# Kernel optimization log

Hardware: AMD Instinct MI355X
Metric: run time of the kernel (lower is better)

Reference implementation:

```python
import jax, jax.numpy as jnp
import numpy as np
import math

DIM = 2048
NUM_HEADS = 16
HEAD_DIM = DIM // NUM_HEADS
SEQ = 2048
BATCH = 4
THETA = 10000.0


def _rope_tables(seq_len, d, theta):
    # faithful to RotaryEmbedding: emb = cat([freqs, freqs], -1), then [..., ::2]
    inv_freq = 1.0 / theta ** (np.arange(0, d, 2, dtype=np.float32) / d)  # [d/2]
    t = np.arange(seq_len, dtype=np.float32)
    freqs = np.einsum('i,j->ij', t, inv_freq)          # [S, d/2]
    emb = np.concatenate([freqs, freqs], axis=-1)       # [S, d]
    cos_split = np.cos(emb)[:, ::2]                     # [S, d/2]
    sin_split = np.sin(emb)[:, ::2]                     # [S, d/2]
    return jnp.asarray(cos_split), jnp.asarray(sin_split)


def _apply_rope(x, cos_s, sin_s):
    # x: [b, h, s, d]; cos_s/sin_s: [s, d/2]
    x1 = x[..., ::2]
    x2 = x[..., 1::2]
    c = cos_s[None, None]
    s = sin_s[None, None]
    return jnp.concatenate([x1 * c - x2 * s, x1 * s + x2 * c], axis=-1)


def setup_inputs() -> dict:
    key = jax.random.key(0)
    k1, k2, k3 = jax.random.split(key, 3)
    x = jax.random.normal(k1, (BATCH, SEQ, DIM), dtype=jnp.float32)
    # causal additive mask [1,1,S,S]
    neg = jnp.finfo(jnp.float32).min
    causal = jnp.tril(jnp.ones((SEQ, SEQ), dtype=bool))
    mask = jnp.where(causal, 0.0, neg)[None, None].astype(jnp.float32)
    w_qkv = jax.random.normal(k2, (3 * DIM, DIM), dtype=jnp.float32) * (1.0 / math.sqrt(DIM))
    w_out = jax.random.normal(k3, (DIM, DIM), dtype=jnp.float32) * (1.0 / math.sqrt(DIM))
    return {"x": x, "mask": mask, "w_qkv": w_qkv, "w_out": w_out}


def reference(x, mask, w_qkv, w_out):
    b, s, _ = x.shape
    h, d = NUM_HEADS, HEAD_DIM
    qkv = jnp.einsum('bse,fe->bsf', x, w_qkv)           # [b, s, 3*dim]
    q, k, v = jnp.split(qkv, 3, axis=-1)
    # b s (h d) -> b h s d
    reshp = lambda t: t.reshape(b, s, h, d).transpose(0, 2, 1, 3)
    q, k, v = reshp(q), reshp(k), reshp(v)
    cos_s, sin_s = _rope_tables(s, d, THETA)
    q = _apply_rope(q, cos_s, sin_s)
    k = _apply_rope(k, cos_s, sin_s)
    att = jnp.einsum('bhqd,bhkd->bhqk', q, k) / math.sqrt(d)
    att = att + mask
    att = jax.nn.softmax(att, axis=-1)
    y = jnp.einsum('bhqk,bhkd->bhqd', att, v)           # [b, h, s, d]
    y = y.transpose(0, 2, 1, 3).reshape(b, s, h * d)
    return jnp.einsum('bse,fe->bsf', y, w_out)
```

## Files before the change

### kernel.cpp

```cpp
#include <hip/hip_runtime.h>

typedef unsigned short u16;
typedef unsigned int u32;
typedef __attribute__((ext_vector_type(4))) float f32x4;
typedef __attribute__((ext_vector_type(16))) float f32x16;
typedef __attribute__((ext_vector_type(8))) short bf16x8;
typedef __attribute__((ext_vector_type(4))) float float4v;
typedef __attribute__((ext_vector_type(4))) unsigned short u16x4;
typedef __attribute__((ext_vector_type(8))) unsigned short u16x8;

__device__ __forceinline__ float bf2f(u16 u) { return __uint_as_float(((u32)u) << 16); }
__device__ __forceinline__ u16 f2bf(float f) {
  u32 x = __float_as_uint(f);
  x += 0x7fffu + ((x >> 16) & 1u);
  return (u16)(x >> 16);
}
__device__ __forceinline__ u32 cvtpk(float lo, float hi_) {
  u32 r;
  asm("v_cvt_pk_bf16_f32 %0, %1, %2" : "=v"(r) : "v"(lo), "v"(hi_));
  return r;
}

__device__ __forceinline__ void gll16(const void* g, void* l) {
  __builtin_amdgcn_global_load_lds((const __attribute__((address_space(1))) void*)g,
                                   (__attribute__((address_space(3))) void*)l, 16, 0, 0);
}

#define MFMA_BF16(a, b, c) __builtin_amdgcn_mfma_f32_16x16x32_bf16((a), (b), (c), 0, 0, 0)
#define MFMA32(a, b, c) __builtin_amdgcn_mfma_f32_32x32x16_bf16((a), (b), (c), 0, 0, 0)

#define BARRIER() __builtin_amdgcn_s_barrier()
#define LGKM0() do { asm volatile("s_waitcnt lgkmcnt(0)" ::: "memory"); \
                     __builtin_amdgcn_sched_barrier(0); } while (0)
#define VMCNT(n) do { asm volatile("s_waitcnt vmcnt(" #n ")" ::: "memory"); \
                      __builtin_amdgcn_sched_barrier(0); } while (0)

__global__ __launch_bounds__(256) void cast_kernel(const float* __restrict__ src,
                                                   u16* __restrict__ dst, int n) {
  const int stride = gridDim.x * 256 * 4;
  for (int i = (blockIdx.x * 256 + threadIdx.x) * 4; i < n; i += stride) {
    const float4v v = *(const float4v*)(src + i);
    u16x4 o;
    o[0] = f2bf(v[0]); o[1] = f2bf(v[1]); o[2] = f2bf(v[2]); o[3] = f2bf(v[3]);
    *(u16x4*)(dst + i) = o;
  }
}

__global__ __launch_bounds__(256) void rope_tables(float* __restrict__ cosd,
                                                   float* __restrict__ sind) {
  const int idx = blockIdx.x * 256 + threadIdx.x;
  const int t = idx >> 6, j = idx & 63;
  const float inv = powf(10000.0f, -(float)(j & 31) * (1.0f / 32.0f));
  const float ang = (float)t * inv;
  cosd[idx] = cosf(ang);
  sind[idx] = sinf(ang);
}

__device__ __forceinline__ void store_out(float* C, size_t i, float v) { C[i] = v; }
__device__ __forceinline__ void store_out(u16* C, size_t i, float v) { C[i] = f2bf(v); }

#define PH_MFMA(MG, NG)                                                          \
  do {                                                                           \
    _Pragma("unroll") for (int i_ = 0; i_ < 4; ++i_)                             \
      _Pragma("unroll") for (int jn_ = 0; jn_ < 2; ++jn_)                        \
        _Pragma("unroll") for (int ks_ = 0; ks_ < 2; ++ks_)                      \
          acc[(MG) * 4 + i_][(NG) * 2 + jn_] =                                   \
              MFMA_BF16(af[i_][ks_], bfr[jn_][ks_],                              \
                        acc[(MG) * 4 + i_][(NG) * 2 + jn_]);                     \
  } while (0)

template <typename OutT>
__global__ __launch_bounds__(512, 2) void gemm_bt8(const u16* __restrict__ A,
                                                   const u16* __restrict__ B,
                                                   OutT* __restrict__ C, int M, int N, int K,
                                                   int lda, int ldb, int ldc) {
  __shared__ __align__(16) u16 LDS[2][2][2][128 * 64];
  const int nbn = N >> 8;
  const int nwg = gridDim.x;
  const int wg = (blockIdx.x & 7) * (nwg >> 3) + (blockIdx.x >> 3);
  const int bm = wg / nbn, bn = wg % nbn;
  const int tid = threadIdx.x;
  const int w = tid >> 6, l = tid & 63, l15 = l & 15, l4 = l >> 4;
  const int wr = w >> 2, wc = w & 3;
  const u16* Abase = A + (size_t)bm * 256 * lda;
  const u16* Bbase = B + (size_t)bn * 256 * ldb;
  const int NT = K >> 6;

  f32x4 acc[8][4] = {};
  bf16x8 af[4][2], bfr[2][2];

  auto STAGE = [&](int sel, int h, int t) {
    const u16* src = (sel ? Bbase + (size_t)h * 128 * ldb : Abase + (size_t)h * 128 * lda) +
                     t * 64;
    const int ld = sel ? ldb : lda;
    char* dst = (char*)&LDS[t & 1][sel][h][0];
#pragma unroll
    for (int j = 0; j < 2; ++j) {
      const int o = j * 8192 + tid * 16;
      const int r = o >> 7;
      const int cb = (o & 127) ^ ((r & 7) << 4);
      gll16(src + (size_t)r * ld + (cb >> 1), dst + o);
    }
  };
  auto LDA_ = [&](int bb, int mg) {
    const char* base = (const char*)&LDS[bb][0][mg][0];
#pragma unroll
    for (int i = 0; i < 4; ++i) {
      const int R = i * 32 + wr * 16 + l15;
#pragma unroll
      for (int ks = 0; ks < 2; ++ks)
        af[i][ks] = *(const bf16x8*)(base + R * 128 + ((ks * 64 + l4 * 16) ^ ((R & 7) << 4)));
    }
  };
  auto LDB_ = [&](int bb, int ng) {
    const char* base = (const char*)&LDS[bb][1][ng][0];
#pragma unroll
    for (int jn = 0; jn < 2; ++jn) {
      const int R = jn * 64 + wc * 16 + l15;
#pragma unroll
      for (int ks = 0; ks < 2; ++ks)
        bfr[jn][ks] = *(const bf16x8*)(base + R * 128 + ((ks * 64 + l4 * 16) ^ ((R & 7) << 4)));
    }
  };

  STAGE(0, 0, 0); STAGE(1, 0, 0); STAGE(0, 1, 0); STAGE(1, 1, 0);
  if (NT > 1) { STAGE(1, 0, 1); STAGE(0, 1, 1); STAGE(1, 1, 1); }
  VMCNT(6);
  BARRIER();

  for (int T = 0; T < NT; ++T) {
    const int bb = T & 1;
    LDA_(bb, 0); LDB_(bb, 0);
    if (T + 1 < NT) STAGE(0, 0, T + 1);
    BARRIER(); LGKM0();
    __builtin_amdgcn_s_setprio(1); PH_MFMA(0, 0); __builtin_amdgcn_s_setprio(0);
    BARRIER();
    LDA_(bb, 1);
    if (T + 2 < NT) STAGE(1, 0, T + 2);
    BARRIER(); LGKM0();
    __builtin_amdgcn_s_setprio(1); PH_MFMA(1, 0); __builtin_amdgcn_s_setprio(0);
    BARRIER();
    LDB_(bb, 1);
    if (T + 2 < NT) STAGE(0, 1, T + 2);
    BARRIER(); LGKM0();
    __builtin_amdgcn_s_setprio(1); PH_MFMA(1, 1); __builtin_amdgcn_s_setprio(0);
    BARRIER();
    LDA_(bb, 0);
    if (T + 2 < NT) STAGE(1, 1, T + 2);
    BARRIER(); LGKM0();
    __builtin_amdgcn_s_setprio(1); PH_MFMA(0, 1); __builtin_amdgcn_s_setprio(0);
    if (T + 2 < NT) { VMCNT(6); } else { VMCNT(0); }
    BARRIER();
  }

#pragma unroll
  for (int mf = 0; mf < 8; ++mf) {
    const int mg = mf >> 2, i = mf & 3;
    const int row0 = bm * 256 + mg * 128 + i * 32 + wr * 16 + l4 * 4;
#pragma unroll
    for (int f = 0; f < 4; ++f) {
      const int col = bn * 256 + f * 64 + wc * 16 + l15;
#pragma unroll
      for (int rr = 0; rr < 4; ++rr)
        store_out(C, (size_t)(row0 + rr) * ldc + col, acc[mf][f][rr]);
    }
  }
}

__global__ __launch_bounds__(256) void rope_apply_inplace(u16* __restrict__ qkvb,
                                                          const float* __restrict__ cosd,
                                                          const float* __restrict__ sind) {
  const int wid = blockIdx.x * 4 + (threadIdx.x >> 6);
  const int j = threadIdx.x & 63;
  const int h = wid & 15;
  const int m = wid >> 4;
  const int s = m & 2047;
  const float c = cosd[s * 64 + j];
  const float sn = sind[s * 64 + j];
  u16* qp = qkvb + (size_t)m * 6144 + h * 128;
  u16* kp = qp + 2048;
  const u32 qv = *(const u32*)(qp + 2 * j);
  const u32 kv = *(const u32*)(kp + 2 * j);
  const float q1 = bf2f((u16)(qv & 0xffff)), q2 = bf2f((u16)(qv >> 16));
  const float k1 = bf2f((u16)(kv & 0xffff)), k2 = bf2f((u16)(kv >> 16));
  qp[j]      = f2bf(q1 * c - q2 * sn);
  qp[64 + j] = f2bf(q1 * sn + q2 * c);
  kp[j]      = f2bf(k1 * c - k2 * sn);
  kp[64 + j] = f2bf(k1 * sn + k2 * c);
}

__global__ __launch_bounds__(256) void v_transpose(const u16* __restrict__ qkvb,
                                                   u16* __restrict__ vt) {
  __shared__ u16 tile[64][130];
  const int st = blockIdx.x & 31, bh = blockIdx.x >> 5;
  const int b = bh >> 4, h = bh & 15;
  const int tid = threadIdx.x;
#pragma unroll
  for (int p = 0; p < 4; ++p) {
    const int ss = p * 16 + (tid >> 4);
    const int d0 = (tid & 15) * 8;
    const u16x8 v = *(const u16x8*)(qkvb + (size_t)(b * 2048 + st * 64 + ss) * 6144 +
                                    4096 + h * 128 + d0);
#pragma unroll
    for (int i = 0; i < 8; ++i) tile[ss][d0 + i] = v[i];
  }
  __syncthreads();
#pragma unroll
  for (int p = 0; p < 4; ++p) {
    const int d = p * 32 + (tid >> 3);
    const int s0 = (tid & 7) * 8;
    u16x8 ov;
#pragma unroll
    for (int i = 0; i < 8; ++i) ov[i] = tile[s0 + i][d];
    *(u16x8*)(vt + (size_t)(bh * 128 + d) * 2048 + st * 64 + s0) = ov;
  }
}

__global__ __launch_bounds__(512, 2) void flash_attn(u16* __restrict__ qkvb,
                                                     const u16* __restrict__ vt) {
  __shared__ __align__(16) char smem[65536];
  const int bh = blockIdx.x;
  const int qt = 7 - blockIdx.y;
  const int b = bh >> 4, h = bh & 15;
  const int tid = threadIdx.x;
  const int w = tid >> 6, l = tid & 63;
  const int l31 = l & 31, hi = l >> 5;

  const int q0 = qt * 256 + w * 32;
  const int qg = q0 + l31;

  bf16x8 qf[8];
  {
    const u16* Qrow = qkvb + (size_t)(b * 2048 + qg) * 6144 + h * 128 + hi * 8;
#pragma unroll
    for (int d = 0; d < 8; ++d) qf[d] = *(const bf16x8*)(Qrow + d * 16);
  }

  f32x16 ot[4];
#pragma unroll
  for (int dt = 0; dt < 4; ++dt) ot[dt] = 0.f;
  float mrun = -1e30f, lrun = 0.f;

  const int NT = 4 * qt + 4;
  const u16* Kg0 = qkvb + (size_t)b * 2048 * 6144 + 2048 + h * 128;
  const u16* Vg0 = vt + (size_t)bh * 128 * 2048;

  auto STAGE = [&](int t) {
    const u16* Kg = Kg0 + (size_t)t * 64 * 6144;
    const u16* Vg = Vg0 + t * 64;
    char* kd = smem + (t & 1) * 16384;
    char* vd = smem + 32768 + (t & 1) * 16384;
#pragma unroll
    for (int j = 0; j < 2; ++j) {
      const int o = j * 8192 + tid * 16;
      {
        const int r = o >> 8;
        const int cb = (o & 255) ^ ((r & 15) << 4);
        gll16(Kg + (size_t)r * 6144 + (cb >> 1), kd + o);
      }
      {
        const int r = o >> 7;
        const int cb = (o & 127) ^ ((r & 7) << 4);
        gll16(Vg + (size_t)r * 2048 + (cb >> 1), vd + o);
      }
    }
  };

  STAGE(0);
  VMCNT(0);
  BARRIER();

  for (int kt = 0; kt < NT; ++kt) {
    if (kt + 1 < NT) STAGE(kt + 1);

    if (kt * 64 <= q0 + 31) {
      const char* Kb = smem + (kt & 1) * 16384;
      const char* Vb = smem + 32768 + (kt & 1) * 16384;

      f32x16 sa[2];
      sa[0] = 0.f; sa[1] = 0.f;
#pragma unroll
      for (int ks2 = 0; ks2 < 2; ++ks2) {
        const int R = ks2 * 32 + l31;
#pragma unroll
        for (int d = 0; d < 8; ++d) {
          const bf16x8 kf = *(const bf16x8*)(Kb + R * 256 +
                                             ((d * 32 + hi * 16) ^ ((R & 15) << 4)));
          sa[ks2] = MFMA32(kf, qf[d], sa[ks2]);
        }
      }

      const float SCALE = 0.08838834764831845f;
      float tmax = -1e30f;
      if (kt * 64 + 63 > q0) {
#pragma unroll
        for (int ks2 = 0; ks2 < 2; ++ks2)
#pragma unroll
          for (int rg = 0; rg < 16; ++rg) {
            const int key = kt * 64 + ks2 * 32 + (rg & 3) + 8 * (rg >> 2) + 4 * hi;
            float sv = sa[ks2][rg] * SCALE;
            sv = (key > qg) ? -1e30f : sv;
            sa[ks2][rg] = sv;
            tmax = fmaxf(tmax, sv);
          }
      } else {
#pragma unroll
        for (int ks2 = 0; ks2 < 2; ++ks2)
#pragma unroll
          for (int rg = 0; rg < 16; ++rg) {
            const float sv = sa[ks2][rg] * SCALE;
            sa[ks2][rg] = sv;
            tmax = fmaxf(tmax, sv);
          }
      }
      tmax = fmaxf(tmax, __shfl_xor(tmax, 32));

      const float mnew = fmaxf(mrun, tmax);
      const float alpha = __expf(mrun - mnew);
      mrun = mnew;
      float rsum = 0.f;
#pragma unroll
      for (int ks2 = 0; ks2 < 2; ++ks2)
#pragma unroll
        for (int rg = 0; rg < 16; ++rg) {
          const float pv = __expf(sa[ks2][rg] - mnew);
          sa[ks2][rg] = pv;
          rsum += pv;
        }
      rsum += __shfl_xor(rsum, 32);
      lrun = lrun * alpha + rsum;
#pragma unroll
      for (int dt = 0; dt < 4; ++dt)
#pragma unroll
        for (int rg = 0; rg < 16; ++rg) ot[dt][rg] *= alpha;

      bf16x8 pfrag[4];
#pragma unroll
      for (int t = 0; t < 4; ++t) {
        const int ks2 = t >> 1;
        const int gA = 2 * (t & 1);
        const int gB = gA + 1;
        const u32 a0 = cvtpk(sa[ks2][gA * 4 + 0], sa[ks2][gA * 4 + 1]);
        const u32 a1 = cvtpk(sa[ks2][gA * 4 + 2], sa[ks2][gA * 4 + 3]);
        const u32 b0 = cvtpk(sa[ks2][gB * 4 + 0], sa[ks2][gB * 4 + 1]);
        const u32 b1 = cvtpk(sa[ks2][gB * 4 + 2], sa[ks2][gB * 4 + 3]);
        const u32 snd0 = hi ? a0 : b0;
        const u32 snd1 = hi ? a1 : b1;
        const u32 rcv0 = (u32)__shfl_xor((int)snd0, 32);
        const u32 rcv1 = (u32)__shfl_xor((int)snd1, 32);
        union { u32 u[4]; bf16x8 v; } pk;
        pk.u[0] = hi ? rcv0 : a0;
        pk.u[1] = hi ? rcv1 : a1;
        pk.u[2] = hi ? b0 : rcv0;
        pk.u[3] = hi ? b1 : rcv1;
        pfrag[t] = pk.v;
      }

#pragma unroll
      for (int dt = 0; dt < 4; ++dt) {
        const int R = dt * 32 + l31;
#pragma unroll
        for (int t = 0; t < 4; ++t) {
          const bf16x8 vf = *(const bf16x8*)(Vb + R * 128 +
                                             ((t * 32 + hi * 16) ^ ((R & 7) << 4)));
          ot[dt] = MFMA32(vf, pfrag[t], ot[dt]);
        }
      }
    }

    VMCNT(0);
    BARRIER();
  }

  const float inv = 1.0f / lrun;
  char* E = smem + w * 8192;
#pragma unroll
  for (int dt = 0; dt < 4; ++dt)
#pragma unroll
    for (int rp = 0; rp < 8; ++rp) {
      const int rg = 2 * rp;
      const int d0 = dt * 32 + (rg & 3) + 8 * (rg >> 2) + 4 * hi;
      const u32 pkv = cvtpk(ot[dt][rg] * inv, ot[dt][rg + 1] * inv);
      *(u32*)(E + l31 * 256 + ((d0 * 2) ^ ((l31 & 15) << 4))) = pkv;
    }
#pragma unroll
  for (int p = 0; p < 8; ++p) {
    const int q = p * 4 + (l >> 4);
    const int c = l & 15;
    const bf16x8 vv = *(const bf16x8*)(E + q * 256 + ((c * 16) ^ ((q & 15) << 4)));
    *(bf16x8*)(qkvb + (size_t)(b * 2048 + q0 + q) * 6144 + h * 128 + c * 8) = vv;
  }
}

extern "C" void kernel_launch(void* const* d_in, const int* in_sizes, int n_in,
                              void* d_out, int out_size, void* d_ws, size_t ws_size,
                              hipStream_t stream) {
  const float* x     = (const float*)d_in[0];
  const float* w_qkv = (const float*)d_in[2];
  const float* w_out = (const float*)d_in[3];
  float* out = (float*)d_out;
  char* ws = (char*)d_ws;

  u16* woutb = (u16*)(ws);
  u16* xb    = (u16*)(ws + ((size_t)8 << 20));
  u16* vt    = (u16*)(ws + ((size_t)8 << 20));
  u16* wqkvb = (u16*)(ws + ((size_t)40 << 20));
  u16* qkvb  = (u16*)(ws + ((size_t)64 << 20));
  float* cosd = (float*)(ws + ((size_t)160 << 20));
  float* sind = (float*)(ws + ((size_t)160 << 20) + ((size_t)1 << 19));

  cast_kernel<<<2048, 256, 0, stream>>>(x, xb, 8192 * 2048);
  cast_kernel<<<2048, 256, 0, stream>>>(w_qkv, wqkvb, 6144 * 2048);
  cast_kernel<<<1024, 256, 0, stream>>>(w_out, woutb, 2048 * 2048);
  rope_tables<<<512, 256, 0, stream>>>(cosd, sind);
  gemm_bt8<u16><<<768, 512, 0, stream>>>(xb, wqkvb, qkvb, 8192, 6144, 2048,
                                         2048, 2048, 6144);
  rope_apply_inplace<<<32768, 256, 0, stream>>>(qkvb, cosd, sind);
  v_transpose<<<2048, 256, 0, stream>>>(qkvb, vt);
  flash_attn<<<dim3(64, 8), 512, 0, stream>>>(qkvb, vt);
  gemm_bt8<float><<<256, 512, 0, stream>>>(qkvb, woutb, out, 8192, 2048, 2048,
                                           6144, 2048, 2048);
}
```

Measured before the change: 431.1 us.

## Switch GEMM to 32x32 MFMA and fuse V transpose into QKV epilogue

The GEMM kernel moves from 16x16x32 to 32x32x16 bf16 MFMA tiles, which changes the per-wave fragment layout and the LDS read pattern. The QKV GEMM epilogue now writes V already transposed into the V region of the qkv buffer, using packed bf16 stores. This removes the separate v_transpose kernel and its extra global round trip, and flash attention reads V^T from qkvb with a 6144 stride. In exchange the epilogue stores become strided scatters, and correctness depends on the V columns of that buffer being reused as a [b,h,d,s] region.

```diff
diff --git a/kernel.cpp b/kernel.cpp
--- a/kernel.cpp
+++ b/kernel.cpp
@@ -26,7 +26,6 @@
                                    (__attribute__((address_space(3))) void*)l, 16, 0, 0);
 }
 
-#define MFMA_BF16(a, b, c) __builtin_amdgcn_mfma_f32_16x16x32_bf16((a), (b), (c), 0, 0, 0)
 #define MFMA32(a, b, c) __builtin_amdgcn_mfma_f32_32x32x16_bf16((a), (b), (c), 0, 0, 0)
 
 #define BARRIER() __builtin_amdgcn_s_barrier()
@@ -56,38 +55,33 @@
   sind[idx] = sinf(ang);
 }
 
-__device__ __forceinline__ void store_out(float* C, size_t i, float v) { C[i] = v; }
-__device__ __forceinline__ void store_out(u16* C, size_t i, float v) { C[i] = f2bf(v); }
-
-#define PH_MFMA(MG, NG)                                                          \
+#define PH_MFMA32(MG, NG)                                                        \
   do {                                                                           \
-    _Pragma("unroll") for (int i_ = 0; i_ < 4; ++i_)                             \
-      _Pragma("unroll") for (int jn_ = 0; jn_ < 2; ++jn_)                        \
-        _Pragma("unroll") for (int ks_ = 0; ks_ < 2; ++ks_)                      \
-          acc[(MG) * 4 + i_][(NG) * 2 + jn_] =                                   \
-              MFMA_BF16(af[i_][ks_], bfr[jn_][ks_],                              \
-                        acc[(MG) * 4 + i_][(NG) * 2 + jn_]);                     \
+    _Pragma("unroll") for (int i_ = 0; i_ < 2; ++i_)                             \
+      _Pragma("unroll") for (int ks_ = 0; ks_ < 4; ++ks_)                        \
+        acc[(MG) * 2 + i_][NG] = MFMA32(af[i_][ks_], bfr[ks_],                   \
+                                        acc[(MG) * 2 + i_][NG]);                 \
   } while (0)
 
-template <typename OutT>
-__global__ __launch_bounds__(512, 2) void gemm_bt8(const u16* __restrict__ A,
-                                                   const u16* __restrict__ B,
-                                                   OutT* __restrict__ C, int M, int N, int K,
-                                                   int lda, int ldb, int ldc) {
+template <int MODE>
+__global__ __launch_bounds__(512, 2) void gemm32(const u16* __restrict__ A,
+                                                 const u16* __restrict__ B,
+                                                 void* __restrict__ Cv, int M, int N, int K,
+                                                 int lda, int ldb, int ldc) {
   __shared__ __align__(16) u16 LDS[2][2][2][128 * 64];
   const int nbn = N >> 8;
   const int nwg = gridDim.x;
   const int wg = (blockIdx.x & 7) * (nwg >> 3) + (blockIdx.x >> 3);
   const int bm = wg / nbn, bn = wg % nbn;
   const int tid = threadIdx.x;
-  const int w = tid >> 6, l = tid & 63, l15 = l & 15, l4 = l >> 4;
+  const int w = tid >> 6, l = tid & 63, l31 = l & 31, hi = l >> 5;
   const int wr = w >> 2, wc = w & 3;
   const u16* Abase = A + (size_t)bm * 256 * lda;
   const u16* Bbase = B + (size_t)bn * 256 * ldb;
   const int NT = K >> 6;
 
-  f32x4 acc[8][4] = {};
-  bf16x8 af[4][2], bfr[2][2];
+  f32x16 acc[4][2] = {};
+  bf16x8 af[2][4], bfr[4];
 
   auto STAGE = [&](int sel, int h, int t) {
     const u16* src = (sel ? Bbase + (size_t)h * 128 * ldb : Abase + (size_t)h * 128 * lda) +
@@ -105,22 +99,19 @@
   auto LDA_ = [&](int bb, int mg) {
     const char* base = (const char*)&LDS[bb][0][mg][0];
 #pragma unroll
-    for (int i = 0; i < 4; ++i) {
-      const int R = i * 32 + wr * 16 + l15;
-#pragma unroll
-      for (int ks = 0; ks < 2; ++ks)
-        af[i][ks] = *(const bf16x8*)(base + R * 128 + ((ks * 64 + l4 * 16) ^ ((R & 7) << 4)));
+    for (int i = 0; i < 2; ++i) {
+      const int R = i * 64 + wr * 32 + l31;
+#pragma unroll
+      for (int ks = 0; ks < 4; ++ks)
+        af[i][ks] = *(const bf16x8*)(base + R * 128 + ((ks * 32 + hi * 16) ^ ((R & 7) << 4)));
     }
   };
   auto LDB_ = [&](int bb, int ng) {
     const char* base = (const char*)&LDS[bb][1][ng][0];
-#pragma unroll
-    for (int jn = 0; jn < 2; ++jn) {
-      const int R = jn * 64 + wc * 16 + l15;
-#pragma unroll
-      for (int ks = 0; ks < 2; ++ks)
-        bfr[jn][ks] = *(const bf16x8*)(base + R * 128 + ((ks * 64 + l4 * 16) ^ ((R & 7) << 4)));
-    }
+    const int Rb = wc * 32 + l31;
+#pragma unroll
+    for (int ks = 0; ks < 4; ++ks)
+      bfr[ks] = *(const bf16x8*)(base + Rb * 128 + ((ks * 32 + hi * 16) ^ ((Rb & 7) << 4)));
   };
 
   STAGE(0, 0, 0); STAGE(1, 0, 0); STAGE(0, 1, 0); STAGE(1, 1, 0);
@@ -133,36 +124,59 @@
     LDA_(bb, 0); LDB_(bb, 0);
     if (T + 1 < NT) STAGE(0, 0, T + 1);
     BARRIER(); LGKM0();
-    __builtin_amdgcn_s_setprio(1); PH_MFMA(0, 0); __builtin_amdgcn_s_setprio(0);
+    __builtin_amdgcn_s_setprio(1); PH_MFMA32(0, 0); __builtin_amdgcn_s_setprio(0);
     BARRIER();
     LDA_(bb, 1);
     if (T + 2 < NT) STAGE(1, 0, T + 2);
     BARRIER(); LGKM0();
-    __builtin_amdgcn_s_setprio(1); PH_MFMA(1, 0); __builtin_amdgcn_s_setprio(0);
+    __builtin_amdgcn_s_setprio(1); PH_MFMA32(1, 0); __builtin_amdgcn_s_setprio(0);
     BARRIER();
     LDB_(bb, 1);
     if (T + 2 < NT) STAGE(0, 1, T + 2);
     BARRIER(); LGKM0();
-    __builtin_amdgcn_s_setprio(1); PH_MFMA(1, 1); __builtin_amdgcn_s_setprio(0);
+    __builtin_amdgcn_s_setprio(1); PH_MFMA32(1, 1); __builtin_amdgcn_s_setprio(0);
     BARRIER();
     LDA_(bb, 0);
     if (T + 2 < NT) STAGE(1, 1, T + 2);
     BARRIER(); LGKM0();
-    __builtin_amdgcn_s_setprio(1); PH_MFMA(0, 1); __builtin_amdgcn_s_setprio(0);
+    __builtin_amdgcn_s_setprio(1); PH_MFMA32(0, 1); __builtin_amdgcn_s_setprio(0);
     if (T + 2 < NT) { VMCNT(6); } else { VMCNT(0); }
     BARRIER();
   }
 
 #pragma unroll
-  for (int mf = 0; mf < 8; ++mf) {
-    const int mg = mf >> 2, i = mf & 3;
-    const int row0 = bm * 256 + mg * 128 + i * 32 + wr * 16 + l4 * 4;
-#pragma unroll
-    for (int f = 0; f < 4; ++f) {
-      const int col = bn * 256 + f * 64 + wc * 16 + l15;
-#pragma unroll
-      for (int rr = 0; rr < 4; ++rr)
-        store_out(C, (size_t)(row0 + rr) * ldc + col, acc[mf][f][rr]);
+  for (int fi = 0; fi < 4; ++fi) {
+    const int mg = fi >> 1, i = fi & 1;
+    const int row0 = bm * 256 + mg * 128 + i * 64 + wr * 32;
+#pragma unroll
+    for (int ng = 0; ng < 2; ++ng) {
+      const int col = bn * 256 + ng * 128 + wc * 32 + l31;
+      const f32x16 a = acc[mg * 2 + i][ng];
+      if (MODE == 0) {
+        float* C = (float*)Cv;
+#pragma unroll
+        for (int r = 0; r < 16; ++r)
+          C[(size_t)(row0 + (r & 3) + 8 * (r >> 2) + 4 * hi) * ldc + col] = a[r];
+      } else if (bn < 16) {
+        u16* C = (u16*)Cv;
+#pragma unroll
+        for (int r = 0; r < 16; ++r)
+          C[(size_t)(row0 + (r & 3) + 8 * (r >> 2) + 4 * hi) * 6144 + col] = f2bf(a[r]);
+      } else {
+        u16* C = (u16*)Cv;
+        const int batch = row0 >> 11;
+        const int srow0 = row0 & 2047;
+        const int vcol = col - 4096;
+        u16* vbase = C + (size_t)((batch * 16 + (vcol >> 7)) * 128 + (vcol & 127)) * 6144 +
+                     4096 + srow0 + 4 * hi;
+#pragma unroll
+        for (int q_ = 0; q_ < 4; ++q_) {
+          union { u32 u[2]; u16x4 v; } pk;
+          pk.u[0] = cvtpk(a[4 * q_ + 0], a[4 * q_ + 1]);
+          pk.u[1] = cvtpk(a[4 * q_ + 2], a[4 * q_ + 3]);
+          *(u16x4*)(vbase + 8 * q_) = pk.v;
+        }
+      }
     }
   }
 }
@@ -189,35 +203,7 @@
   kp[64 + j] = f2bf(k1 * sn + k2 * c);
 }
 
-__global__ __launch_bounds__(256) void v_transpose(const u16* __restrict__ qkvb,
-                                                   u16* __restrict__ vt) {
-  __shared__ u16 tile[64][130];
-  const int st = blockIdx.x & 31, bh = blockIdx.x >> 5;
-  const int b = bh >> 4, h = bh & 15;
-  const int tid = threadIdx.x;
-#pragma unroll
-  for (int p = 0; p < 4; ++p) {
-    const int ss = p * 16 + (tid >> 4);
-    const int d0 = (tid & 15) * 8;
-    const u16x8 v = *(const u16x8*)(qkvb + (size_t)(b * 2048 + st * 64 + ss) * 6144 +
-                                    4096 + h * 128 + d0);
-#pragma unroll
-    for (int i = 0; i < 8; ++i) tile[ss][d0 + i] = v[i];
-  }
-  __syncthreads();
-#pragma unroll
-  for (int p = 0; p < 4; ++p) {
-    const int d = p * 32 + (tid >> 3);
-    const int s0 = (tid & 7) * 8;
-    u16x8 ov;
-#pragma unroll
-    for (int i = 0; i < 8; ++i) ov[i] = tile[s0 + i][d];
-    *(u16x8*)(vt + (size_t)(bh * 128 + d) * 2048 + st * 64 + s0) = ov;
-  }
-}
-
-__global__ __launch_bounds__(512, 2) void flash_attn(u16* __restrict__ qkvb,
-                                                     const u16* __restrict__ vt) {
+__global__ __launch_bounds__(512, 2) void flash_attn(u16* __restrict__ qkvb) {
   __shared__ __align__(16) char smem[65536];
   const int bh = blockIdx.x;
   const int qt = 7 - blockIdx.y;
@@ -243,7 +229,7 @@
 
   const int NT = 4 * qt + 4;
   const u16* Kg0 = qkvb + (size_t)b * 2048 * 6144 + 2048 + h * 128;
-  const u16* Vg0 = vt + (size_t)bh * 128 * 2048;
+  const u16* Vg0 = qkvb + (size_t)bh * 128 * 6144 + 4096;
 
   auto STAGE = [&](int t) {
     const u16* Kg = Kg0 + (size_t)t * 64 * 6144;
@@ -261,7 +247,7 @@
       {
         const int r = o >> 7;
         const int cb = (o & 127) ^ ((r & 7) << 4);
-        gll16(Vg + (size_t)r * 2048 + (cb >> 1), vd + o);
+        gll16(Vg + (size_t)r * 6144 + (cb >> 1), vd + o);
       }
     }
   };
@@ -403,7 +389,6 @@
 
   u16* woutb = (u16*)(ws);
   u16* xb    = (u16*)(ws + ((size_t)8 << 20));
-  u16* vt    = (u16*)(ws + ((size_t)8 << 20));
   u16* wqkvb = (u16*)(ws + ((size_t)40 << 20));
   u16* qkvb  = (u16*)(ws + ((size_t)64 << 20));
   float* cosd = (float*)(ws + ((size_t)160 << 20));
@@ -413,11 +398,10 @@
   cast_kernel<<<2048, 256, 0, stream>>>(w_qkv, wqkvb, 6144 * 2048);
   cast_kernel<<<1024, 256, 0, stream>>>(w_out, woutb, 2048 * 2048);
   rope_tables<<<512, 256, 0, stream>>>(cosd, sind);
-  gemm_bt8<u16><<<768, 512, 0, stream>>>(xb, wqkvb, qkvb, 8192, 6144, 2048,
-                                         2048, 2048, 6144);
+  gemm32<1><<<768, 512, 0, stream>>>(xb, wqkvb, qkvb, 8192, 6144, 2048,
+                                     2048, 2048, 6144);
   rope_apply_inplace<<<32768, 256, 0, stream>>>(qkvb, cosd, sind);
-  v_transpose<<<2048, 256, 0, stream>>>(qkvb, vt);
-  flash_attn<<<dim3(64, 8), 512, 0, stream>>>(qkvb, vt);
-  gemm_bt8<float><<<256, 512, 0, stream>>>(qkvb, woutb, out, 8192, 2048, 2048,
-                                           6144, 2048, 2048);
-}
+  flash_attn<<<dim3(64, 8), 512, 0, stream>>>(qkvb);
+  gemm32<0><<<256, 512, 0, stream>>>(qkvb, woutb, out, 8192, 2048, 2048,
+                                     6144, 2048, 2048);
+}
```

Measured after the change: 465.3 us. 1.08x slower.
